# Performance work log

Measured on AMD Instinct MI355X. Metric: run time of the kernel, lower is better.

The kernel has to match this reference:

```python
import jax, jax.numpy as jnp
import numpy as np


def dht(x):
    # Discrete Hartley transform over spatial dims via FFT (ortho norm):
    # H(x) = Re(F(x)) - Im(F(x)). With norm='ortho' the DHT is its own inverse.
    X = jnp.fft.fftn(x, axes=(2, 3), norm='ortho')
    return X.real - X.imag


def _neg_freq(a):
    # H[-k] = roll(flip(H), 1) along both spectral dims
    return jnp.roll(jnp.flip(a, axis=(-2, -1)), shift=(1, 1), axis=(-2, -1))


def compl_mul2d(x1, x2):
    x1n = _neg_freq(x1)
    x2n = _neg_freq(x2)
    return 0.5 * (
        jnp.einsum('bixy,ioxy->boxy', x1, x2)
        - jnp.einsum('bixy,ioxy->boxy', x1n, x2n)
        + jnp.einsum('bixy,ioxy->boxy', x1, x2n)
        + jnp.einsum('bixy,ioxy->boxy', x1n, x2)
    )


def setup_inputs() -> dict:
    key = jax.random.key(0)
    k1, k2 = jax.random.split(key)
    B, Ci, Co, S, M = 16, 32, 32, 256, 16
    x = jax.random.normal(k1, (B, Ci, S, S), dtype=jnp.float32)
    scale = 1.0 / (Ci * Co)
    weights1 = scale * jax.random.uniform(k2, (Ci, Co, M, M), dtype=jnp.float32)
    return {'x': x, 'weights1': weights1}


def reference(x, weights1):
    B = x.shape[0]
    S1, S2 = x.shape[-2], x.shape[-1]
    Co = weights1.shape[1]
    m1, m2 = weights1.shape[2], weights1.shape[3]
    x_ht = dht(x)                                   # [B, Ci, S1, S2]
    res = compl_mul2d(x_ht[:, :, :m1, :m2], weights1)  # [B, Co, m1, m2]
    out_ht = jnp.zeros((B, Co, S1, S2), dtype=x.dtype).at[:, :, :m1, :m2].set(res)
    return dht(out_ht)                              # inverse DHT == DHT (ortho)
```

## Files before the change

### kernel.cpp

```cpp
#include <hip/hip_runtime.h>

#define SDIM 256
#define MDIM 16
#define CI 32
#define CO 32

constexpr float INV_S = 1.0f / 256.0f;
constexpr float TWO_PI_OVER_S = 6.28318530717958647692f / 256.0f;

__device__ __forceinline__ float4 f4zero() { return make_float4(0.f, 0.f, 0.f, 0.f); }

__device__ __forceinline__ void fma4(float4& a, float x, const float4 w) {
  a.x = fmaf(x, w.x, a.x);
  a.y = fmaf(x, w.y, a.y);
  a.z = fmaf(x, w.z, a.z);
  a.w = fmaf(x, w.w, a.w);
}

__global__ __launch_bounds__(256, 2) void k_fwd(const float* __restrict__ x,
                                                float* __restrict__ xh) {
  __shared__ __align__(16) float cT[SDIM][MDIM];
  __shared__ __align__(16) float sT[SDIM][MDIM];
  __shared__ float C1[MDIM][SDIM];
  __shared__ float S1[MDIM][SDIM];

  const int t = threadIdx.x;

  #pragma unroll
  for (int k = 0; k < MDIM; ++k) {
    float sv, cv;
    sincosf(TWO_PI_OVER_S * (float)((k * t) & 255), &sv, &cv);
    cT[t][k] = cv;
    sT[t][k] = sv;
  }
  __syncthreads();

  const float* __restrict__ xp = x + (size_t)blockIdx.x * (SDIM * SDIM);

  float4 aC[4], aS[4];
  #pragma unroll
  for (int jj = 0; jj < 4; ++jj) { aC[jj] = f4zero(); aS[jj] = f4zero(); }

  {
    float x0 = xp[t];
    float xm = xp[128 * SDIM + t];
    float e = x0 + xm;
    float od = x0 - xm;
    #pragma unroll
    for (int jj = 0; jj < 4; ++jj) {
      aC[jj].x += e; aC[jj].y += od; aC[jj].z += e; aC[jj].w += od;
    }
  }

  for (int base = 1; base + 8 <= 128; base += 8) {
    float xlo[8], xhi[8];
    #pragma unroll
    for (int j = 0; j < 8; ++j) {
      xlo[j] = xp[(base + j) * SDIM + t];
      xhi[j] = xp[(SDIM - base - j) * SDIM + t];
    }
    #pragma unroll
    for (int j = 0; j < 8; ++j) {
      const int n = base + j;
      float es = xlo[j] + xhi[j];
      float ds = xlo[j] - xhi[j];
      const float4* c4 = (const float4*)(&cT[n][0]);
      const float4* s4 = (const float4*)(&sT[n][0]);
      #pragma unroll
      for (int jj = 0; jj < 4; ++jj) {
        fma4(aC[jj], es, c4[jj]);
        fma4(aS[jj], ds, s4[jj]);
      }
    }
  }
  #pragma unroll
  for (int n = 121; n < 128; ++n) {
    float lo = xp[n * SDIM + t];
    float hi = xp[(SDIM - n) * SDIM + t];
    float es = lo + hi, ds = lo - hi;
    const float4* c4 = (const float4*)(&cT[n][0]);
    const float4* s4 = (const float4*)(&sT[n][0]);
    #pragma unroll
    for (int jj = 0; jj < 4; ++jj) {
      fma4(aC[jj], es, c4[jj]);
      fma4(aS[jj], ds, s4[jj]);
    }
  }

  #pragma unroll
  for (int jj = 0; jj < 4; ++jj) {
    C1[4 * jj + 0][t] = aC[jj].x; C1[4 * jj + 1][t] = aC[jj].y;
    C1[4 * jj + 2][t] = aC[jj].z; C1[4 * jj + 3][t] = aC[jj].w;
    S1[4 * jj + 0][t] = aS[jj].x; S1[4 * jj + 1][t] = aS[jj].y;
    S1[4 * jj + 2][t] = aS[jj].z; S1[4 * jj + 3][t] = aS[jj].w;
  }
  __syncthreads();

  const int k1 = t >> 4;
  const int k2 = t & 15;
  float acc = 0.f;
  #pragma unroll 8
  for (int n2 = 0; n2 < SDIM; ++n2) {
    float cv = cT[n2][k2];
    float sv = sT[n2][k2];
    acc = fmaf(C1[k1][n2], cv + sv, acc);
    acc = fmaf(S1[k1][n2], cv - sv, acc);
  }
  xh[(size_t)blockIdx.x * 256 + t] = acc * INV_S;
}

__global__ __launch_bounds__(256, 2) void k_mix(const float* __restrict__ xh,
                                                const float* __restrict__ w,
                                                float* __restrict__ res) {
  __shared__ float xs[CI][256];
  __shared__ float wsm[CI][256];
  const int t = threadIdx.x;
  const int b = blockIdx.x >> 5;
  const int o = blockIdx.x & 31;

  for (int i = 0; i < CI; ++i) {
    xs[i][t] = xh[((size_t)(b * CI + i)) * 256 + t];
    wsm[i][t] = w[((size_t)(i * CO + o)) * 256 + t];
  }
  __syncthreads();

  const int k1 = t >> 4, k2 = t & 15;
  const int tn = (((MDIM - k1) & 15) << 4) | ((MDIM - k2) & 15);
  float acc = 0.f;
  #pragma unroll 8
  for (int i = 0; i < CI; ++i) {
    float xp = xs[i][t], xn = xs[i][tn];
    float wp = wsm[i][t], wn = wsm[i][tn];
    acc = fmaf(xp, wp + wn, acc);
    acc = fmaf(xn, wp - wn, acc);
  }
  res[(size_t)blockIdx.x * 256 + t] = 0.5f * acc;
}

__global__ __launch_bounds__(256, 2) void k_inv(const float* __restrict__ res,
                                               float* __restrict__ out) {
  __shared__ __align__(16) float rs[256];
  __shared__ __align__(16) float U[SDIM][MDIM];
  __shared__ __align__(16) float V[SDIM][MDIM];
  const int t = threadIdx.x;

  rs[t] = res[(size_t)blockIdx.x * 256 + t];

  float ct[16], st[16];
  #pragma unroll
  for (int k = 0; k < 16; ++k) {
    sincosf(TWO_PI_OVER_S * (float)((k * t) & 255), &st[k], &ct[k]);
  }
  __syncthreads();

  {
    float4 u[4], v[4];
    #pragma unroll
    for (int jj = 0; jj < 4; ++jj) { u[jj] = f4zero(); v[jj] = f4zero(); }
    #pragma unroll
    for (int kk1 = 0; kk1 < 16; ++kk1) {
      const float4* r4 = (const float4*)(&rs[kk1 * 16]);
      float c = ct[kk1], s = st[kk1];
      #pragma unroll
      for (int jj = 0; jj < 4; ++jj) {
        float4 r = r4[jj];
        fma4(u[jj], c, r);
        fma4(v[jj], s, r);
      }
    }
    float4* U4 = (float4*)(&U[t][0]);
    float4* V4 = (float4*)(&V[t][0]);
    #pragma unroll
    for (int jj = 0; jj < 4; ++jj) { U4[jj] = u[jj]; V4[jj] = v[jj]; }
  }
  __syncthreads();

  float cp[16], cm[16];
  #pragma unroll
  for (int k = 0; k < 16; ++k) { cp[k] = ct[k] + st[k]; cm[k] = ct[k] - st[k]; }

  float* __restrict__ op = out + (size_t)blockIdx.x * (SDIM * SDIM) + t;
  #pragma unroll 2
  for (int n1 = 0; n1 < SDIM; ++n1) {
    const float4* U4 = (const float4*)(&U[n1][0]);
    const float4* V4 = (const float4*)(&V[n1][0]);
    float acc = 0.f;
    #pragma unroll
    for (int jj = 0; jj < 4; ++jj) {
      float4 uu = U4[jj], vv = V4[jj];
      acc = fmaf(uu.x, cp[4 * jj + 0], acc); acc = fmaf(vv.x, cm[4 * jj + 0], acc);
      acc = fmaf(uu.y, cp[4 * jj + 1], acc); acc = fmaf(vv.y, cm[4 * jj + 1], acc);
      acc = fmaf(uu.z, cp[4 * jj + 2], acc); acc = fmaf(vv.z, cm[4 * jj + 2], acc);
      acc = fmaf(uu.w, cp[4 * jj + 3], acc); acc = fmaf(vv.w, cm[4 * jj + 3], acc);
    }
    op[n1 * SDIM] = acc * INV_S;
  }
}

extern "C" void kernel_launch(void* const* d_in, const int* in_sizes, int n_in,
                              void* d_out, int out_size, void* d_ws, size_t ws_size,
                              hipStream_t stream) {
  const float* x = (const float*)d_in[0];
  const float* w = (const float*)d_in[1];
  float* out = (float*)d_out;

  float* xh  = (float*)d_ws;
  float* res = (float*)d_ws + 512 * 256;

  k_fwd<<<16 * CI, 256, 0, stream>>>(x, xh);
  k_mix<<<16 * CO, 256, 0, stream>>>(xh, w, res);
  k_inv<<<16 * CO, 256, 0, stream>>>(res, out);
}
```

Before: 302.2 us.

## Precompute twiddle tables, scalar-load them, fuse mix with first inverse pass, exploit symmetry

Twiddle tables are computed once by a new tiny kernel into workspace. The forward kernel reads them through scalar s_load_dwordx16 inline asm, which removes the per-block sincos and the shared-memory table traffic. The spectral mix is fused with the first inverse DHT stage, so only the n1 in 0..128 rows are produced. The final inverse kernel uses cos/sin symmetry to write rows n and 256-n from one computation and splits each image across two blocks. The trade-offs are an extra launch, and inline asm that waits for every scalar load with s_waitcnt 0, which serialises load latency.

```diff
diff --git a/kernel.cpp b/kernel.cpp
--- a/kernel.cpp
+++ b/kernel.cpp
@@ -1,199 +1,211 @@
 #include <hip/hip_runtime.h>
 
-#define SDIM 256
-#define MDIM 16
 #define CI 32
 #define CO 32
 
 constexpr float INV_S = 1.0f / 256.0f;
-constexpr float TWO_PI_OVER_S = 6.28318530717958647692f / 256.0f;
-
-__device__ __forceinline__ float4 f4zero() { return make_float4(0.f, 0.f, 0.f, 0.f); }
-
-__device__ __forceinline__ void fma4(float4& a, float x, const float4 w) {
-  a.x = fmaf(x, w.x, a.x);
-  a.y = fmaf(x, w.y, a.y);
-  a.z = fmaf(x, w.z, a.z);
-  a.w = fmaf(x, w.w, a.w);
+constexpr float THETA = 6.28318530717958647692f / 256.0f;
+
+typedef float f32x16 __attribute__((ext_vector_type(16)));
+
+__device__ __forceinline__ f32x16 sload16(const float* p) {
+  f32x16 r;
+  asm volatile("s_load_dwordx16 %0, %1, 0x0\n\ts_waitcnt lgkmcnt(0)"
+               : "=&s"(r) : "s"(p));
+  return r;
+}
+
+__device__ __forceinline__ void sload2x16_64(const float* p, f32x16& a, f32x16& b) {
+  asm volatile("s_load_dwordx16 %0, %2, 0x0\n\t"
+               "s_load_dwordx16 %1, %2, 0x40\n\t"
+               "s_waitcnt lgkmcnt(0)"
+               : "=&s"(a), "=&s"(b) : "s"(p));
+}
+
+__device__ __forceinline__ void sload2x16_16k(const float* p, f32x16& a, f32x16& b) {
+  asm volatile("s_load_dwordx16 %0, %2, 0x0\n\t"
+               "s_load_dwordx16 %1, %2, 0x4000\n\t"
+               "s_waitcnt lgkmcnt(0)"
+               : "=&s"(a), "=&s"(b) : "s"(p));
+}
+
+__global__ void k_tab(float* __restrict__ TCb, float* __restrict__ TSb,
+                      float* __restrict__ TPb, float* __restrict__ TMb) {
+  const int t = threadIdx.x;
+  #pragma unroll
+  for (int k = 0; k < 16; ++k) {
+    float s, c;
+    sincosf(THETA * (float)((k * t) & 255), &s, &c);
+    TCb[t * 16 + k] = c;
+    TSb[t * 16 + k] = s;
+    TPb[k * 256 + t] = c + s;
+    TMb[k * 256 + t] = c - s;
+  }
 }
 
 __global__ __launch_bounds__(256, 2) void k_fwd(const float* __restrict__ x,
+                                                const float* __restrict__ TCb,
+                                                const float* __restrict__ TPb,
+                                                const float* __restrict__ TMb,
                                                 float* __restrict__ xh) {
-  __shared__ __align__(16) float cT[SDIM][MDIM];
-  __shared__ __align__(16) float sT[SDIM][MDIM];
-  __shared__ float C1[MDIM][SDIM];
-  __shared__ float S1[MDIM][SDIM];
-
-  const int t = threadIdx.x;
-
-  #pragma unroll
-  for (int k = 0; k < MDIM; ++k) {
-    float sv, cv;
-    sincosf(TWO_PI_OVER_S * (float)((k * t) & 255), &sv, &cv);
-    cT[t][k] = cv;
-    sT[t][k] = sv;
-  }
-  __syncthreads();
-
-  const float* __restrict__ xp = x + (size_t)blockIdx.x * (SDIM * SDIM);
-
-  float4 aC[4], aS[4];
-  #pragma unroll
-  for (int jj = 0; jj < 4; ++jj) { aC[jj] = f4zero(); aS[jj] = f4zero(); }
-
+  __shared__ __align__(16) float C1[16][260];
+  __shared__ __align__(16) float S1[16][260];
+  const int t = threadIdx.x;
+  const float* __restrict__ xp = x + (size_t)blockIdx.x * 65536 + t;
+
+  float aC[16], aS[16];
   {
-    float x0 = xp[t];
-    float xm = xp[128 * SDIM + t];
-    float e = x0 + xm;
-    float od = x0 - xm;
-    #pragma unroll
-    for (int jj = 0; jj < 4; ++jj) {
-      aC[jj].x += e; aC[jj].y += od; aC[jj].z += e; aC[jj].w += od;
-    }
-  }
-
-  for (int base = 1; base + 8 <= 128; base += 8) {
+    float x0 = xp[0];
+    float xm = xp[128 * 256];
+    float e = x0 + xm, o = x0 - xm;
+    #pragma unroll
+    for (int k = 0; k < 16; ++k) { aC[k] = (k & 1) ? o : e; aS[k] = 0.f; }
+  }
+
+  for (int base = 1; base + 8 <= 121; base += 8) {
     float xlo[8], xhi[8];
     #pragma unroll
     for (int j = 0; j < 8; ++j) {
-      xlo[j] = xp[(base + j) * SDIM + t];
-      xhi[j] = xp[(SDIM - base - j) * SDIM + t];
+      xlo[j] = xp[(base + j) * 256];
+      xhi[j] = xp[(256 - base - j) * 256];
     }
     #pragma unroll
     for (int j = 0; j < 8; ++j) {
       const int n = base + j;
+      f32x16 tc, ts;
+      sload2x16_16k(TCb + n * 16, tc, ts);
       float es = xlo[j] + xhi[j];
       float ds = xlo[j] - xhi[j];
-      const float4* c4 = (const float4*)(&cT[n][0]);
-      const float4* s4 = (const float4*)(&sT[n][0]);
       #pragma unroll
-      for (int jj = 0; jj < 4; ++jj) {
-        fma4(aC[jj], es, c4[jj]);
-        fma4(aS[jj], ds, s4[jj]);
+      for (int k = 0; k < 16; ++k) {
+        aC[k] = fmaf(es, tc[k], aC[k]);
+        aS[k] = fmaf(ds, ts[k], aS[k]);
       }
     }
   }
+  for (int n = 121; n < 128; ++n) {
+    float lo = xp[n * 256];
+    float hi = xp[(256 - n) * 256];
+    f32x16 tc, ts;
+    sload2x16_16k(TCb + n * 16, tc, ts);
+    float es = lo + hi, ds = lo - hi;
+    #pragma unroll
+    for (int k = 0; k < 16; ++k) {
+      aC[k] = fmaf(es, tc[k], aC[k]);
+      aS[k] = fmaf(ds, ts[k], aS[k]);
+    }
+  }
+
   #pragma unroll
-  for (int n = 121; n < 128; ++n) {
-    float lo = xp[n * SDIM + t];
-    float hi = xp[(SDIM - n) * SDIM + t];
-    float es = lo + hi, ds = lo - hi;
-    const float4* c4 = (const float4*)(&cT[n][0]);
-    const float4* s4 = (const float4*)(&sT[n][0]);
-    #pragma unroll
-    for (int jj = 0; jj < 4; ++jj) {
-      fma4(aC[jj], es, c4[jj]);
-      fma4(aS[jj], ds, s4[jj]);
-    }
-  }
-
-  #pragma unroll
-  for (int jj = 0; jj < 4; ++jj) {
-    C1[4 * jj + 0][t] = aC[jj].x; C1[4 * jj + 1][t] = aC[jj].y;
-    C1[4 * jj + 2][t] = aC[jj].z; C1[4 * jj + 3][t] = aC[jj].w;
-    S1[4 * jj + 0][t] = aS[jj].x; S1[4 * jj + 1][t] = aS[jj].y;
-    S1[4 * jj + 2][t] = aS[jj].z; S1[4 * jj + 3][t] = aS[jj].w;
-  }
+  for (int k = 0; k < 16; ++k) { C1[k][t] = aC[k]; S1[k][t] = aS[k]; }
   __syncthreads();
 
-  const int k1 = t >> 4;
-  const int k2 = t & 15;
+  const int k1 = t >> 4, k2 = t & 15;
+  const float* __restrict__ tp = TPb + k2 * 256;
+  const float* __restrict__ tm = TMb + k2 * 256;
   float acc = 0.f;
-  #pragma unroll 8
-  for (int n2 = 0; n2 < SDIM; ++n2) {
-    float cv = cT[n2][k2];
-    float sv = sT[n2][k2];
-    acc = fmaf(C1[k1][n2], cv + sv, acc);
-    acc = fmaf(S1[k1][n2], cv - sv, acc);
+  #pragma unroll 2
+  for (int n2 = 0; n2 < 256; n2 += 4) {
+    const float4 c4 = *(const float4*)&C1[k1][n2];
+    const float4 s4 = *(const float4*)&S1[k1][n2];
+    const float4 p4 = *(const float4*)&tp[n2];
+    const float4 m4 = *(const float4*)&tm[n2];
+    acc = fmaf(c4.x, p4.x, acc); acc = fmaf(s4.x, m4.x, acc);
+    acc = fmaf(c4.y, p4.y, acc); acc = fmaf(s4.y, m4.y, acc);
+    acc = fmaf(c4.z, p4.z, acc); acc = fmaf(s4.z, m4.z, acc);
+    acc = fmaf(c4.w, p4.w, acc); acc = fmaf(s4.w, m4.w, acc);
   }
   xh[(size_t)blockIdx.x * 256 + t] = acc * INV_S;
 }
 
-__global__ __launch_bounds__(256, 2) void k_mix(const float* __restrict__ xh,
+__global__ __launch_bounds__(256, 2) void k_mid(const float* __restrict__ xh,
                                                 const float* __restrict__ w,
-                                                float* __restrict__ res) {
+                                                float* __restrict__ Wout) {
   __shared__ float xs[CI][256];
-  __shared__ float wsm[CI][256];
+  __shared__ __align__(16) float rsm[256];
   const int t = threadIdx.x;
   const int b = blockIdx.x >> 5;
   const int o = blockIdx.x & 31;
 
-  for (int i = 0; i < CI; ++i) {
-    xs[i][t] = xh[((size_t)(b * CI + i)) * 256 + t];
-    wsm[i][t] = w[((size_t)(i * CO + o)) * 256 + t];
-  }
+  #pragma unroll 8
+  for (int i = 0; i < CI; ++i)
+    xs[i][t] = xh[(size_t)(b * CI + i) * 256 + t];
   __syncthreads();
 
   const int k1 = t >> 4, k2 = t & 15;
-  const int tn = (((MDIM - k1) & 15) << 4) | ((MDIM - k2) & 15);
+  const int tn = (((16 - k1) & 15) << 4) | ((16 - k2) & 15);
   float acc = 0.f;
   #pragma unroll 8
   for (int i = 0; i < CI; ++i) {
-    float xp = xs[i][t], xn = xs[i][tn];
-    float wp = wsm[i][t], wn = wsm[i][tn];
-    acc = fmaf(xp, wp + wn, acc);
-    acc = fmaf(xn, wp - wn, acc);
-  }
-  res[(size_t)blockIdx.x * 256 + t] = 0.5f * acc;
-}
-
-__global__ __launch_bounds__(256, 2) void k_inv(const float* __restrict__ res,
-                                               float* __restrict__ out) {
-  __shared__ __align__(16) float rs[256];
-  __shared__ __align__(16) float U[SDIM][MDIM];
-  __shared__ __align__(16) float V[SDIM][MDIM];
-  const int t = threadIdx.x;
-
-  rs[t] = res[(size_t)blockIdx.x * 256 + t];
-
-  float ct[16], st[16];
+    const float* __restrict__ wrow = w + (size_t)(i * CO + o) * 256;
+    float wp = wrow[t];
+    float wn = wrow[tn];
+    float xv = xs[i][t];
+    float xnv = xs[i][tn];
+    acc = fmaf(xv, wp + wn, acc);
+    acc = fmaf(xnv, wp - wn, acc);
+  }
+  rsm[t] = 0.5f * acc;
+  __syncthreads();
+
+  if (t <= 128) {
+    float cc[16], ssn[16];
+    #pragma unroll
+    for (int k = 0; k < 16; ++k)
+      sincosf(THETA * (float)((k * t) & 255), &ssn[k], &cc[k]);
+    float U[16], V[16];
+    #pragma unroll
+    for (int j = 0; j < 16; ++j) { U[j] = 0.f; V[j] = 0.f; }
+    #pragma unroll
+    for (int kk1 = 0; kk1 < 16; ++kk1) {
+      float c = cc[kk1], s = ssn[kk1];
+      #pragma unroll
+      for (int j = 0; j < 16; ++j) {
+        float r = rsm[kk1 * 16 + j];
+        U[j] = fmaf(c, r, U[j]);
+        V[j] = fmaf(s, r, V[j]);
+      }
+    }
+    float* __restrict__ wr = Wout + (size_t)blockIdx.x * 4128 + t * 32;
+    #pragma unroll
+    for (int j = 0; j < 16; ++j) {
+      wr[j] = U[j] * INV_S;
+      wr[16 + j] = V[j] * INV_S;
+    }
+  }
+}
+
+__global__ __launch_bounds__(256, 4) void k_invB(const float* __restrict__ Wb,
+                                                 float* __restrict__ out) {
+  const int t = threadIdx.x;
+  const int img = blockIdx.x >> 1;
+  const int half = blockIdx.x & 1;
+
+  float cp[16], cm[16];
   #pragma unroll
   for (int k = 0; k < 16; ++k) {
-    sincosf(TWO_PI_OVER_S * (float)((k * t) & 255), &st[k], &ct[k]);
-  }
-  __syncthreads();
-
-  {
-    float4 u[4], v[4];
-    #pragma unroll
-    for (int jj = 0; jj < 4; ++jj) { u[jj] = f4zero(); v[jj] = f4zero(); }
-    #pragma unroll
-    for (int kk1 = 0; kk1 < 16; ++kk1) {
-      const float4* r4 = (const float4*)(&rs[kk1 * 16]);
-      float c = ct[kk1], s = st[kk1];
-      #pragma unroll
-      for (int jj = 0; jj < 4; ++jj) {
-        float4 r = r4[jj];
-        fma4(u[jj], c, r);
-        fma4(v[jj], s, r);
-      }
-    }
-    float4* U4 = (float4*)(&U[t][0]);
-    float4* V4 = (float4*)(&V[t][0]);
-    #pragma unroll
-    for (int jj = 0; jj < 4; ++jj) { U4[jj] = u[jj]; V4[jj] = v[jj]; }
-  }
-  __syncthreads();
-
-  float cp[16], cm[16];
-  #pragma unroll
-  for (int k = 0; k < 16; ++k) { cp[k] = ct[k] + st[k]; cm[k] = ct[k] - st[k]; }
-
-  float* __restrict__ op = out + (size_t)blockIdx.x * (SDIM * SDIM) + t;
-  #pragma unroll 2
-  for (int n1 = 0; n1 < SDIM; ++n1) {
-    const float4* U4 = (const float4*)(&U[n1][0]);
-    const float4* V4 = (const float4*)(&V[n1][0]);
-    float acc = 0.f;
-    #pragma unroll
-    for (int jj = 0; jj < 4; ++jj) {
-      float4 uu = U4[jj], vv = V4[jj];
-      acc = fmaf(uu.x, cp[4 * jj + 0], acc); acc = fmaf(vv.x, cm[4 * jj + 0], acc);
-      acc = fmaf(uu.y, cp[4 * jj + 1], acc); acc = fmaf(vv.y, cm[4 * jj + 1], acc);
-      acc = fmaf(uu.z, cp[4 * jj + 2], acc); acc = fmaf(vv.z, cm[4 * jj + 2], acc);
-      acc = fmaf(uu.w, cp[4 * jj + 3], acc); acc = fmaf(vv.w, cm[4 * jj + 3], acc);
-    }
-    op[n1 * SDIM] = acc * INV_S;
+    float s, c;
+    sincosf(THETA * (float)((k * t) & 255), &s, &c);
+    cp[k] = c + s;
+    cm[k] = c - s;
+  }
+
+  const float* __restrict__ wbase = Wb + (size_t)img * 4128;
+  float* __restrict__ op = out + (size_t)img * 65536 + t;
+
+  const int n_lo = half ? 65 : 0;
+  const int n_hi = half ? 128 : 64;
+  for (int n = n_lo; n <= n_hi; ++n) {
+    f32x16 uu, vv;
+    sload2x16_64(wbase + n * 32, uu, vv);
+    float a = 0.f, bsum = 0.f;
+    #pragma unroll
+    for (int k = 0; k < 16; ++k) {
+      a = fmaf(uu[k], cp[k], a);
+      bsum = fmaf(vv[k], cm[k], bsum);
+    }
+    op[(size_t)n * 256] = a + bsum;
+    if (n >= 1 && n <= 127) op[(size_t)(256 - n) * 256] = a - bsum;
   }
 }
 
@@ -204,10 +216,15 @@
   const float* w = (const float*)d_in[1];
   float* out = (float*)d_out;
 
-  float* xh  = (float*)d_ws;
-  float* res = (float*)d_ws + 512 * 256;
-
-  k_fwd<<<16 * CI, 256, 0, stream>>>(x, xh);
-  k_mix<<<16 * CO, 256, 0, stream>>>(xh, w, res);
-  k_inv<<<16 * CO, 256, 0, stream>>>(res, out);
-}
+  float* TCb = (float*)d_ws;
+  float* TSb = TCb + 4096;
+  float* TPb = TSb + 4096;
+  float* TMb = TPb + 4096;
+  float* xh  = TMb + 4096;
+  float* Wb  = xh + 131072;
+
+  k_tab<<<1, 256, 0, stream>>>(TCb, TSb, TPb, TMb);
+  k_fwd<<<16 * CI, 256, 0, stream>>>(x, TCb, TPb, TMb, xh);
+  k_mid<<<16 * CO, 256, 0, stream>>>(xh, w, Wb);
+  k_invB<<<2 * 16 * CO, 256, 0, stream>>>(Wb, out);
+}
```

New measurement: 308.5 us. 2.1% more time.
